# Optimization experiments

Measured on AMD Instinct MI355X. Metric: run time of the kernel, lower is better.

Reference implementation:

```python
import jax, jax.numpy as jnp
import numpy as np

B, DIN, DOUT, E, H, K = 8192, 1024, 1024, 8, 128, 2

def setup_inputs() -> dict:
    key = jax.random.key(0)
    ks = jax.random.split(key, 6)
    s = 0.02
    return {
        "x": jax.random.normal(ks[0], (B, DIN), jnp.float32),
        "w1": jax.random.normal(ks[1], (DIN, H), jnp.float32) * s,
        "b1": jnp.zeros((H,), jnp.float32),
        "wg": jax.random.normal(ks[2], (DIN, H), jnp.float32) * s,
        "bg": jnp.zeros((H,), jnp.float32),
        "w2": jax.random.normal(ks[3], (H, E), jnp.float32) * s,
        "b2": jnp.zeros((E,), jnp.float32),
        "we": jax.random.normal(ks[4], (E, DIN, DOUT), jnp.float32) * s,
        "be": jnp.zeros((E, DOUT), jnp.float32),
    }

def reference(x, w1, b1, wg, bg, w2, b2, we, be):
    Bx = x.shape[0]
    Eo = we.shape[0]
    Do = we.shape[2]
    # Router with GLU; NOTE: softmax over BATCH dim (dim=0), as in source.
    h = (x @ w1 + b1) * jax.nn.relu(x @ wg + bg)
    h = jax.nn.relu(h)
    l = jax.nn.softmax(x=(h @ w2 + b2), axis=0)  # [B, E]
    batch_K = -(-K * Bx) // Eo  # ceil(K/E * B), static
    # top-k tokens per expert (along batch dim)
    ws_t, ib_t = jax.lax.top_k(l.T, batch_K)  # [E, bK]
    ws, ib = ws_t.T, ib_t.T                   # [bK, E]
    nws = jax.nn.softmax(ws, axis=0)          # renorm over selected tokens
    # dispatch: gather selected tokens for all experts at once
    sel = x[ib]                                # [bK, E, DIN]
    eo = jnp.einsum('ked,edo->keo', sel, we) + be  # [bK, E, DOUT]
    eo = eo * nws[:, :, None]
    # combine (concat_sum): per-expert scatter-set + shared scatter-add sum
    e_idx = jnp.broadcast_to(jnp.arange(Eo)[None, :], ib.shape)  # [bK, E]
    out_e = jnp.zeros((Eo, Bx, Do), x.dtype).at[e_idx, ib].set(eo)
    temp_sum = jnp.zeros((Bx, Do), x.dtype).at[ib].add(eo)
    out_e = out_e + temp_sum[None]
    return out_e.transpose(1, 0, 2).reshape(Bx, Eo * Do)
```

## Files before the change

kernel.cpp:

```cpp
#include <hip/hip_runtime.h>
#include <math.h>

#define B_TOK 8192
#define D_IN 1024
#define D_OUT 1024
#define N_E 8
#define N_H 128
#define SEL 2048

using bf16x8 = __attribute__((ext_vector_type(8))) short;
using floatx4 = __attribute__((ext_vector_type(4))) float;

__device__ __forceinline__ unsigned short f2bf(float f) {
  unsigned u = __float_as_uint(f);
  u = (u + 0x7FFFu + ((u >> 16) & 1u)) >> 16;
  return (unsigned short)u;
}

__device__ __forceinline__ float bf2f(unsigned short h) {
  return __uint_as_float(((unsigned)h) << 16);
}

__device__ __forceinline__ void async_cp16(const void* g, void* l) {
  __builtin_amdgcn_global_load_lds((__attribute__((address_space(1))) void*)g,
                                   (__attribute__((address_space(3))) void*)l,
                                   16, 0, 0);
}

__global__ __launch_bounds__(256) void k_router_fat(const float* __restrict__ x,
                                                    const float* __restrict__ w1,
                                                    const float* __restrict__ b1,
                                                    const float* __restrict__ wg,
                                                    const float* __restrict__ bg,
                                                    const float* __restrict__ w2,
                                                    const float* __restrict__ b2,
                                                    const float* __restrict__ we,
                                                    unsigned short* __restrict__ xb,
                                                    double* __restrict__ logits,
                                                    unsigned short* __restrict__ web) {
  __shared__ char smem[39168];
  const int t = threadIdx.x;

  if (blockIdx.x >= 512) {
    const int wb = blockIdx.x - 512;
    const int e = wb >> 8;
    const int rem = wb & 255;
    const int o0 = (rem >> 4) * 64;
    const int d0 = (rem & 15) * 64;
    float (*tile)[68] = (float(*)[68])smem;
    const float* wsrc = we + (size_t)e * D_IN * D_OUT;
    unsigned short* wdst = web + (size_t)e * D_OUT * D_IN;
    const int r = t >> 4;
    const int c = (t & 15) * 4;
#pragma unroll
    for (int p = 0; p < 4; ++p) {
      float4 v = *(const float4*)(wsrc + (size_t)(d0 + r + 16 * p) * D_OUT + o0 + c);
      tile[r + 16 * p][c] = v.x; tile[r + 16 * p][c + 1] = v.y;
      tile[r + 16 * p][c + 2] = v.z; tile[r + 16 * p][c + 3] = v.w;
    }
    __syncthreads();
#pragma unroll
    for (int p = 0; p < 4; ++p) {
      int orow = r + 16 * p;
      ushort4 v;
      v.x = f2bf(tile[c + 0][orow]); v.y = f2bf(tile[c + 1][orow]);
      v.z = f2bf(tile[c + 2][orow]); v.w = f2bf(tile[c + 3][orow]);
      *(ushort4*)(wdst + (size_t)(o0 + orow) * D_IN + d0 + c) = v;
    }
    return;
  }

  float (*xs)[36]  = (float(*)[36])(smem);
  float (*ws1)[128] = (float(*)[128])(smem + 2304);
  float (*wsg)[128] = (float(*)[128])(smem + 2304 + 16384);
  float* w2s = (float*)(smem + 2304 + 16384 + 16384);
  const int b0 = blockIdx.x * 16;
  const int tg = t >> 5;
  const int og = t & 31;

  ((float4*)w2s)[t] = ((const float4*)w2)[t];

  double d1[2][4] = {}; double dg[2][4] = {};
  for (int k0 = 0; k0 < D_IN; k0 += 32) {
    __syncthreads();
    if (t < 128) {
      int r = t >> 3, c = (t & 7) * 4;
      float4 v = *(const float4*)(x + (size_t)(b0 + r) * D_IN + k0 + c);
      *(float4*)(&xs[r][c]) = v;
      ushort4 u; u.x = f2bf(v.x); u.y = f2bf(v.y); u.z = f2bf(v.z); u.w = f2bf(v.w);
      *(ushort4*)(xb + (size_t)(b0 + r) * D_IN + k0 + c) = u;
    }
    {
      int r = t >> 5, c = (t & 31) * 4;
#pragma unroll
      for (int p = 0; p < 4; ++p) {
        *(float4*)(&ws1[r + 8 * p][c]) = *(const float4*)(w1 + (size_t)(k0 + r + 8 * p) * N_H + c);
        *(float4*)(&wsg[r + 8 * p][c]) = *(const float4*)(wg + (size_t)(k0 + r + 8 * p) * N_H + c);
      }
    }
    __syncthreads();
    float a1[2][4] = {}; float ag[2][4] = {};
    for (int k = 0; k < 32; k += 4) {
      float xk[2][4];
#pragma unroll
      for (int i = 0; i < 2; ++i) {
        float4 v = *(const float4*)(&xs[tg * 2 + i][k]);
        xk[i][0] = v.x; xk[i][1] = v.y; xk[i][2] = v.z; xk[i][3] = v.w;
      }
#pragma unroll
      for (int kk = 0; kk < 4; ++kk) {
        float4 w1v = *(const float4*)(&ws1[k + kk][og * 4]);
        float4 wgv = *(const float4*)(&wsg[k + kk][og * 4]);
        float wa1[4] = {w1v.x, w1v.y, w1v.z, w1v.w};
        float wag[4] = {wgv.x, wgv.y, wgv.z, wgv.w};
#pragma unroll
        for (int i = 0; i < 2; ++i) {
#pragma unroll
          for (int j = 0; j < 4; ++j) {
            a1[i][j] += xk[i][kk] * wa1[j];
            ag[i][j] += xk[i][kk] * wag[j];
          }
        }
      }
    }
#pragma unroll
    for (int i = 0; i < 2; ++i)
#pragma unroll
      for (int j = 0; j < 4; ++j) { d1[i][j] += a1[i][j]; dg[i][j] += ag[i][j]; }
  }

  float4 b1v = *(const float4*)(b1 + og * 4);
  float4 bgv = *(const float4*)(bg + og * 4);
  float b1a[4] = {b1v.x, b1v.y, b1v.z, b1v.w};
  float bga[4] = {bgv.x, bgv.y, bgv.z, bgv.w};
  float hv[2][4];
#pragma unroll
  for (int i = 0; i < 2; ++i) {
#pragma unroll
    for (int j = 0; j < 4; ++j) {
      float a = (float)d1[i][j] + b1a[j];
      float g = (float)dg[i][j] + bga[j];
      g = fmaxf(g, 0.f);
      hv[i][j] = fmaxf(a * g, 0.f);
    }
  }

  double lp[2][8] = {};
#pragma unroll
  for (int i = 0; i < 2; ++i) {
#pragma unroll
    for (int j = 0; j < 4; ++j) {
      double hj = (double)hv[i][j];
      int kk = og * 4 + j;
#pragma unroll
      for (int e = 0; e < 8; ++e)
        lp[i][e] += hj * (double)w2s[kk * N_E + e];
    }
  }
#pragma unroll
  for (int o = 16; o; o >>= 1) {
#pragma unroll
    for (int i = 0; i < 2; ++i)
#pragma unroll
      for (int e = 0; e < 8; ++e)
        lp[i][e] += __shfl_down(lp[i][e], o);
  }
  if (og == 0) {
#pragma unroll
    for (int i = 0; i < 2; ++i)
#pragma unroll
      for (int e = 0; e < 8; ++e)
        logits[(size_t)(b0 + tg * 2 + i) * N_E + e] = lp[i][e] + (double)b2[e];
  }
}

__global__ __launch_bounds__(256) void k_topk(const double* __restrict__ logits,
                                              int* __restrict__ ib, float* __restrict__ nws,
                                              int* __restrict__ slot) {
  const int e = blockIdx.x;
  const int t = threadIdx.x;
  __shared__ double redd[4];
  __shared__ int redi[4];
  __shared__ unsigned redu[4];
  __shared__ int s_cnt;

  double lv[32];
#pragma unroll
  for (int i = 0; i < 32; ++i) lv[i] = logits[(size_t)(t + i * 256) * N_E + e];

  double m = -1e300;
#pragma unroll
  for (int i = 0; i < 32; ++i) m = fmax(m, lv[i]);
  for (int o = 32; o; o >>= 1) m = fmax(m, __shfl_down(m, o));
  __syncthreads();
  if ((t & 63) == 0) redd[t >> 6] = m;
  __syncthreads();
  const double maxl = fmax(fmax(redd[0], redd[1]), fmax(redd[2], redd[3]));

  double s = 0.0;
#pragma unroll
  for (int i = 0; i < 32; ++i) s += exp(lv[i] - maxl);
  for (int o = 32; o; o >>= 1) s += __shfl_down(s, o);
  __syncthreads();
  if ((t & 63) == 0) redd[t >> 6] = s;
  __syncthreads();
  const double sum = redd[0] + redd[1] + redd[2] + redd[3];

  unsigned kr[32];
#pragma unroll
  for (int i = 0; i < 32; ++i) {
    float lf = (float)(exp(lv[i] - maxl) / sum);
    kr[i] = __float_as_uint(lf);
  }

  unsigned mnk = 0xFFFFFFFFu, mxk = 0;
#pragma unroll
  for (int i = 0; i < 32; ++i) { mnk = (kr[i] < mnk) ? kr[i] : mnk; mxk = (kr[i] > mxk) ? kr[i] : mxk; }
  for (int o = 32; o; o >>= 1) {
    unsigned v = __shfl_down(mnk, o); mnk = (v < mnk) ? v : mnk;
    unsigned w = __shfl_down(mxk, o); mxk = (w > mxk) ? w : mxk;
  }
  __syncthreads();
  if ((t & 63) == 0) redu[t >> 6] = mnk;
  __syncthreads();
  mnk = redu[0]; if (redu[1] < mnk) mnk = redu[1]; if (redu[2] < mnk) mnk = redu[2]; if (redu[3] < mnk) mnk = redu[3];
  __syncthreads();
  if ((t & 63) == 0) redu[t >> 6] = mxk;
  __syncthreads();
  mxk = redu[0]; if (redu[1] > mxk) mxk = redu[1]; if (redu[2] > mxk) mxk = redu[2]; if (redu[3] > mxk) mxk = redu[3];

  const unsigned diff = mnk ^ mxk;
  int hb = -1;
  unsigned thr;
  if (diff == 0) {
    thr = mnk;
  } else {
    hb = 31 - __clz(diff);
    thr = mxk & ~((hb >= 31) ? 0xFFFFFFFFu : ((1u << (hb + 1)) - 1u));
  }

  for (int bit = hb; bit >= 0; --bit) {
    unsigned trial = thr | (1u << bit);
    int c = 0;
#pragma unroll
    for (int i = 0; i < 32; ++i) c += (kr[i] >= trial) ? 1 : 0;
    for (int o = 32; o; o >>= 1) c += __shfl_down(c, o);
    __syncthreads();
    if ((t & 63) == 0) redi[t >> 6] = c;
    __syncthreads();
    c = redi[0] + redi[1] + redi[2] + redi[3];
    if (c >= SEL) thr = trial;
  }

  int c1 = 0, ceq = 0;
#pragma unroll
  for (int i = 0; i < 32; ++i) {
    c1 += (kr[i] > thr) ? 1 : 0;
    ceq += (kr[i] == thr) ? 1 : 0;
  }
  for (int o = 32; o; o >>= 1) { c1 += __shfl_down(c1, o); ceq += __shfl_down(ceq, o); }
  __syncthreads();
  if ((t & 63) == 0) { redi[t >> 6] = c1; ((int*)redu)[t >> 6] = ceq; }
  __syncthreads();
  c1 = redi[0] + redi[1] + redi[2] + redi[3];
  ceq = ((int*)redu)[0] + ((int*)redu)[1] + ((int*)redu)[2] + ((int*)redu)[3];
  const int need = SEL - c1;

  int cut;
  if (ceq == need) {
    cut = B_TOK;
  } else {
    cut = 0;
    for (int bit = 12; bit >= 0; --bit) {
      int trial = cut | (1 << bit);
      int c = 0;
#pragma unroll
      for (int i = 0; i < 32; ++i) c += (kr[i] == thr && (t + i * 256) < trial) ? 1 : 0;
      for (int o = 32; o; o >>= 1) c += __shfl_down(c, o);
      __syncthreads();
      if ((t & 63) == 0) redi[t >> 6] = c;
      __syncthreads();
      c = redi[0] + redi[1] + redi[2] + redi[3];
      if (c < need) cut = trial;
    }
  }

  const double maxw = (double)__uint_as_float(mxk);

  double ss = 0.0;
#pragma unroll
  for (int i = 0; i < 32; ++i) {
    int idx = t + i * 256;
    bool sel = (kr[i] > thr) || (kr[i] == thr && idx <= cut);
    if (sel) ss += exp((double)__uint_as_float(kr[i]) - maxw);
  }
  for (int o = 32; o; o >>= 1) ss += __shfl_down(ss, o);
  __syncthreads();
  if ((t & 63) == 0) redd[t >> 6] = ss;
  __syncthreads();
  const double ssum = redd[0] + redd[1] + redd[2] + redd[3];

  if (t == 0) s_cnt = 0;
#pragma unroll
  for (int i = 0; i < 32; ++i) slot[(size_t)(t + i * 256) * N_E + e] = -1;
  __syncthreads();
  for (int i = 0; i < 32; ++i) {
    int idx = t + i * 256;
    bool sel = (kr[i] > thr) || (kr[i] == thr && idx <= cut);
    if (sel) {
      int pos = atomicAdd(&s_cnt, 1);
      ib[e * SEL + pos] = idx;
      nws[e * SEL + pos] = (float)(exp((double)__uint_as_float(kr[i]) - maxw) / ssum);
      slot[(size_t)idx * N_E + e] = pos;
    }
  }
}

__global__ __launch_bounds__(256) void k_expert_gemm(const unsigned short* __restrict__ xb,
                                                     const unsigned short* __restrict__ web,
                                                     const float* __restrict__ be,
                                                     const int* __restrict__ ib,
                                                     const float* __restrict__ nws,
                                                     unsigned short* __restrict__ eo) {
  __shared__ unsigned short As[128 * 64];
  __shared__ unsigned short Bs[128 * 64];
  __shared__ int rowidx[128];
  __shared__ float nwss[128];
  const int e = blockIdx.z;
  const int bm = blockIdx.x * 128;
  const int bn = blockIdx.y * 128;
  const int t = threadIdx.x;
  const int wave = t >> 6, lane = t & 63;
  if (t < 128) {
    rowidx[t] = ib[e * SEL + bm + t];
    nwss[t] = nws[e * SEL + bm + t];
  }
  __syncthreads();
  const unsigned short* wbase = web + (size_t)e * D_IN * D_OUT;
  const int chunk = lane & 7;
  const unsigned short* aptr[4];
  const unsigned short* bptr[4];
  unsigned short* adst[4];
  unsigned short* bdst[4];
#pragma unroll
  for (int c = 0; c < 4; ++c) {
    int row = c * 32 + wave * 8 + (lane >> 3);
    aptr[c] = xb + (size_t)rowidx[row] * D_IN + chunk * 8;
    bptr[c] = wbase + (size_t)(bn + row) * D_IN + chunk * 8;
    adst[c] = As + row * 64 + chunk * 8;
    bdst[c] = Bs + row * 64 + chunk * 8;
  }
  floatx4 acc[4][4] = {};
  const int wm = wave >> 1, wn = wave & 1;
  const int fr = lane & 15, fq = lane >> 4;

  for (int k0 = 0; k0 < D_IN; k0 += 64) {
#pragma unroll
    for (int c = 0; c < 4; ++c) {
      async_cp16(aptr[c] + k0, adst[c]);
      async_cp16(bptr[c] + k0, bdst[c]);
    }
    __syncthreads();
#pragma unroll
    for (int kk = 0; kk < 2; ++kk) {
      bf16x8 af[4], bfr[4];
#pragma unroll
      for (int mt = 0; mt < 4; ++mt)
        af[mt] = *(const bf16x8*)(As + (wm * 64 + mt * 16 + fr) * 64 + kk * 32 + fq * 8);
#pragma unroll
      for (int nt = 0; nt < 4; ++nt)
        bfr[nt] = *(const bf16x8*)(Bs + (wn * 64 + nt * 16 + fr) * 64 + kk * 32 + fq * 8);
#pragma unroll
      for (int mt = 0; mt < 4; ++mt)
#pragma unroll
        for (int nt = 0; nt < 4; ++nt)
          acc[mt][nt] = __builtin_amdgcn_mfma_f32_16x16x32_bf16(af[mt], bfr[nt], acc[mt][nt], 0, 0, 0);
    }
    __syncthreads();
  }
  float bev[4];
#pragma unroll
  for (int nt = 0; nt < 4; ++nt) bev[nt] = be[e * D_OUT + bn + wn * 64 + nt * 16 + fr];
#pragma unroll
  for (int mt = 0; mt < 4; ++mt) {
#pragma unroll
    for (int r = 0; r < 4; ++r) {
      int lrow = wm * 64 + mt * 16 + fq * 4 + r;
      float nw = nwss[lrow];
      size_t rbase = ((size_t)e * SEL + bm + lrow) * D_OUT;
#pragma unroll
      for (int nt = 0; nt < 4; ++nt) {
        int cc = bn + wn * 64 + nt * 16 + fr;
        eo[rbase + cc] = f2bf((acc[mt][nt][r] + bev[nt]) * nw);
      }
    }
  }
}

__global__ __launch_bounds__(256) void k_combine(const unsigned short* __restrict__ eo,
                                                 const int* __restrict__ slot,
                                                 float* __restrict__ out) {
  const int b = blockIdx.x;
  const int t = threadIdx.x;
  __shared__ int ss[8];
  if (t < 8) ss[t] = slot[(size_t)b * N_E + t];
  __syncthreads();
  const int d0 = t * 4;
  float vx[8], vy[8], vz[8], vw[8];
  float tx = 0.f, ty = 0.f, tz = 0.f, tw = 0.f;
#pragma unroll
  for (int e = 0; e < 8; ++e) {
    int k = ss[e];
    if (k >= 0) {
      ushort4 u = *(const ushort4*)(eo + ((size_t)e * SEL + k) * D_OUT + d0);
      vx[e] = bf2f(u.x); vy[e] = bf2f(u.y); vz[e] = bf2f(u.z); vw[e] = bf2f(u.w);
      tx += vx[e]; ty += vy[e]; tz += vz[e]; tw += vw[e];
    } else {
      vx[e] = 0.f; vy[e] = 0.f; vz[e] = 0.f; vw[e] = 0.f;
    }
  }
#pragma unroll
  for (int e = 0; e < 8; ++e) {
    float4 o;
    o.x = tx + vx[e]; o.y = ty + vy[e]; o.z = tz + vz[e]; o.w = tw + vw[e];
    *(float4*)(out + (size_t)b * (N_E * D_OUT) + e * D_OUT + d0) = o;
  }
}

extern "C" void kernel_launch(void* const* d_in, const int* in_sizes, int n_in,
                              void* d_out, int out_size, void* d_ws, size_t ws_size,
                              hipStream_t stream) {
  const float* x  = (const float*)d_in[0];
  const float* w1 = (const float*)d_in[1];
  const float* b1 = (const float*)d_in[2];
  const float* wg = (const float*)d_in[3];
  const float* bg = (const float*)d_in[4];
  const float* w2 = (const float*)d_in[5];
  const float* b2 = (const float*)d_in[6];
  const float* we = (const float*)d_in[7];
  const float* be = (const float*)d_in[8];
  float* out = (float*)d_out;

  char* ws = (char*)d_ws;
  size_t off = 0;
  auto alloc = [&](size_t bytes) -> void* {
    void* p = ws + off;
    off += (bytes + 255) & ~(size_t)255;
    return p;
  };
  unsigned short* xb  = (unsigned short*)alloc((size_t)B_TOK * D_IN * 2);
  unsigned short* web = (unsigned short*)alloc((size_t)N_E * D_IN * D_OUT * 2);
  unsigned short* eo  = (unsigned short*)alloc((size_t)N_E * SEL * D_OUT * 2);
  double* lgts  = (double*)alloc((size_t)B_TOK * N_E * 8);
  int* ibuf     = (int*)alloc((size_t)N_E * SEL * 4);
  float* nws    = (float*)alloc((size_t)N_E * SEL * 4);
  int* slot     = (int*)alloc((size_t)B_TOK * N_E * 4);
  if (off > ws_size) return;

  hipLaunchKernelGGL(k_router_fat, dim3(512 + 2048), dim3(256), 0, stream,
                     x, w1, b1, wg, bg, w2, b2, we, xb, lgts, web);
  hipLaunchKernelGGL(k_topk, dim3(N_E), dim3(256), 0, stream, lgts, ibuf, nws, slot);
  hipLaunchKernelGGL(k_expert_gemm, dim3(SEL / 128, D_OUT / 128, N_E), dim3(256), 0, stream,
                     xb, web, be, ibuf, nws, eo);
  hipLaunchKernelGGL(k_combine, dim3(B_TOK), dim3(256), 0, stream, eo, slot, out);
}
```

Baseline: 516.3 us.

## Double-buffer expert GEMM with 256x256 tiles, swizzled LDS and prioritised MFMA

```diff
diff --git a/kernel.cpp b/kernel.cpp
--- a/kernel.cpp
+++ b/kernel.cpp
@@ -316,81 +316,104 @@
   }
 }
 
-__global__ __launch_bounds__(256) void k_expert_gemm(const unsigned short* __restrict__ xb,
-                                                     const unsigned short* __restrict__ web,
-                                                     const float* __restrict__ be,
-                                                     const int* __restrict__ ib,
-                                                     const float* __restrict__ nws,
-                                                     unsigned short* __restrict__ eo) {
-  __shared__ unsigned short As[128 * 64];
-  __shared__ unsigned short Bs[128 * 64];
-  __shared__ int rowidx[128];
-  __shared__ float nwss[128];
+__global__ __launch_bounds__(512, 2) void k_expert_gemm(const unsigned short* __restrict__ xb,
+                                                        const unsigned short* __restrict__ web,
+                                                        const float* __restrict__ be,
+                                                        const int* __restrict__ ib,
+                                                        const float* __restrict__ nws,
+                                                        unsigned short* __restrict__ eo) {
+  __shared__ unsigned short S[2 * 32768];
+  __shared__ int rowidx[256];
+  __shared__ float nwss[256];
   const int e = blockIdx.z;
-  const int bm = blockIdx.x * 128;
-  const int bn = blockIdx.y * 128;
+  const int bm = blockIdx.x * 256;
+  const int bn = blockIdx.y * 256;
   const int t = threadIdx.x;
   const int wave = t >> 6, lane = t & 63;
-  if (t < 128) {
+  if (t < 256) {
     rowidx[t] = ib[e * SEL + bm + t];
     nwss[t] = nws[e * SEL + bm + t];
   }
   __syncthreads();
   const unsigned short* wbase = web + (size_t)e * D_IN * D_OUT;
-  const int chunk = lane & 7;
-  const unsigned short* aptr[4];
-  const unsigned short* bptr[4];
-  unsigned short* adst[4];
-  unsigned short* bdst[4];
-#pragma unroll
-  for (int c = 0; c < 4; ++c) {
-    int row = c * 32 + wave * 8 + (lane >> 3);
-    aptr[c] = xb + (size_t)rowidx[row] * D_IN + chunk * 8;
-    bptr[c] = wbase + (size_t)(bn + row) * D_IN + chunk * 8;
-    adst[c] = As + row * 64 + chunk * 8;
-    bdst[c] = Bs + row * 64 + chunk * 8;
-  }
-  floatx4 acc[4][4] = {};
-  const int wm = wave >> 1, wn = wave & 1;
+
+  const unsigned short* asrc[4];
+  const unsigned short* bsrc[4];
+  int adst[4], bdst[4];
+#pragma unroll
+  for (int j = 0; j < 4; ++j) {
+    int idx = t + j * 512;
+    int r = idx >> 3;
+    int c16 = (idx & 7) ^ (r & 7);
+    asrc[j] = xb + (size_t)rowidx[r] * D_IN + c16 * 8;
+    adst[j] = idx * 8;
+    bsrc[j] = wbase + (size_t)(bn + r) * D_IN + c16 * 8;
+    bdst[j] = 16384 + idx * 8;
+  }
+
+#define STAGE(kt, buf)                                                        \
+  {                                                                           \
+    _Pragma("unroll")                                                         \
+    for (int j = 0; j < 4; ++j) {                                             \
+      async_cp16(asrc[j] + (kt) * 64, S + (buf) * 32768 + adst[j]);           \
+      async_cp16(bsrc[j] + (kt) * 64, S + (buf) * 32768 + bdst[j]);           \
+    }                                                                         \
+  }
+
+  floatx4 acc[8][4] = {};
+  const int wr = wave >> 2, wc = wave & 3;
   const int fr = lane & 15, fq = lane >> 4;
-
-  for (int k0 = 0; k0 < D_IN; k0 += 64) {
-#pragma unroll
-    for (int c = 0; c < 4; ++c) {
-      async_cp16(aptr[c] + k0, adst[c]);
-      async_cp16(bptr[c] + k0, bdst[c]);
-    }
-    __syncthreads();
+  const int swz = (fr & 7) << 3;
+
+  STAGE(0, 0);
+  STAGE(1, 1);
+
+  for (int kt = 0; kt < 16; ++kt) {
+    const int cur = kt & 1;
+    if (kt == 15) {
+      asm volatile("s_waitcnt vmcnt(0)" ::: "memory");
+    } else {
+      asm volatile("s_waitcnt vmcnt(8)" ::: "memory");
+    }
+    __builtin_amdgcn_s_barrier();
+    const unsigned short* Ab = S + cur * 32768;
+    const unsigned short* Bb = Ab + 16384;
+    __builtin_amdgcn_s_setprio(1);
 #pragma unroll
     for (int kk = 0; kk < 2; ++kk) {
-      bf16x8 af[4], bfr[4];
-#pragma unroll
-      for (int mt = 0; mt < 4; ++mt)
-        af[mt] = *(const bf16x8*)(As + (wm * 64 + mt * 16 + fr) * 64 + kk * 32 + fq * 8);
+      bf16x8 af[8], bfr[4];
+#pragma unroll
+      for (int mt = 0; mt < 8; ++mt)
+        af[mt] = *(const bf16x8*)(Ab + (wr * 128 + mt * 16 + fr) * 64 + ((kk * 32 + fq * 8) ^ swz));
 #pragma unroll
       for (int nt = 0; nt < 4; ++nt)
-        bfr[nt] = *(const bf16x8*)(Bs + (wn * 64 + nt * 16 + fr) * 64 + kk * 32 + fq * 8);
-#pragma unroll
-      for (int mt = 0; mt < 4; ++mt)
+        bfr[nt] = *(const bf16x8*)(Bb + (wc * 64 + nt * 16 + fr) * 64 + ((kk * 32 + fq * 8) ^ swz));
+#pragma unroll
+      for (int mt = 0; mt < 8; ++mt)
 #pragma unroll
         for (int nt = 0; nt < 4; ++nt)
           acc[mt][nt] = __builtin_amdgcn_mfma_f32_16x16x32_bf16(af[mt], bfr[nt], acc[mt][nt], 0, 0, 0);
     }
-    __syncthreads();
-  }
+    __builtin_amdgcn_s_setprio(0);
+    __builtin_amdgcn_sched_barrier(0);
+    __builtin_amdgcn_s_barrier();
+    if (kt < 14) STAGE(kt + 2, cur);
+  }
+#undef STAGE
+
   float bev[4];
 #pragma unroll
-  for (int nt = 0; nt < 4; ++nt) bev[nt] = be[e * D_OUT + bn + wn * 64 + nt * 16 + fr];
-#pragma unroll
-  for (int mt = 0; mt < 4; ++mt) {
+  for (int nt = 0; nt < 4; ++nt) bev[nt] = be[e * D_OUT + bn + wc * 64 + nt * 16 + fr];
+#pragma unroll
+  for (int mt = 0; mt < 8; ++mt) {
 #pragma unroll
     for (int r = 0; r < 4; ++r) {
-      int lrow = wm * 64 + mt * 16 + fq * 4 + r;
+      int lrow = wr * 128 + mt * 16 + fq * 4 + r;
       float nw = nwss[lrow];
       size_t rbase = ((size_t)e * SEL + bm + lrow) * D_OUT;
 #pragma unroll
       for (int nt = 0; nt < 4; ++nt) {
-        int cc = bn + wn * 64 + nt * 16 + fr;
+        int cc = bn + wc * 64 + nt * 16 + fr;
         eo[rbase + cc] = f2bf((acc[mt][nt][r] + bev[nt]) * nw);
       }
     }
@@ -460,7 +483,7 @@
   hipLaunchKernelGGL(k_router_fat, dim3(512 + 2048), dim3(256), 0, stream,
                      x, w1, b1, wg, bg, w2, b2, we, xb, lgts, web);
   hipLaunchKernelGGL(k_topk, dim3(N_E), dim3(256), 0, stream, lgts, ibuf, nws, slot);
-  hipLaunchKernelGGL(k_expert_gemm, dim3(SEL / 128, D_OUT / 128, N_E), dim3(256), 0, stream,
+  hipLaunchKernelGGL(k_expert_gemm, dim3(SEL / 256, D_OUT / 256, N_E), dim3(512), 0, stream,
                      xb, web, be, ibuf, nws, eo);
   hipLaunchKernelGGL(k_combine, dim3(B_TOK), dim3(256), 0, stream, eo, slot, out);
 }
```

Result: faster. 503.5 us (-2.5%).
